# Kernel optimization log

Hardware: AMD Instinct MI355X
Metric: run time of the kernel (lower is better)

The kernel has to match this reference:

```python
import jax, jax.numpy as jnp
import numpy as np

B, T, S, C, E, H = 4, 2048, 2048, 256, 512, 8
D = E // H
SCALE = E ** (-0.5)


def setup_inputs() -> dict:
    key = jax.random.key(0)
    ks = jax.random.split(key, 12)
    x = jax.random.normal(ks[0], (B, T, C), dtype=jnp.float32)
    context = jax.random.normal(ks[1], (B, S, E), dtype=jnp.float32)
    pad_mask = jax.random.randint(ks[2], (B, T, S), 0, 2) == 1
    p = 0.02
    # Conv1d kernel_size=1 weights stored squeezed: [out_ch, in_ch]
    w_in = jax.random.normal(ks[3], (E, C), dtype=jnp.float32) * p
    b_in = jnp.zeros((E,), dtype=jnp.float32)
    wq = jax.random.normal(ks[4], (E, E), dtype=jnp.float32) * p
    bq = jnp.zeros((E,), dtype=jnp.float32)
    wk = jax.random.normal(ks[5], (E, E), dtype=jnp.float32) * p
    bk = jnp.zeros((E,), dtype=jnp.float32)
    wv = jax.random.normal(ks[6], (E, E), dtype=jnp.float32) * p
    bv = jnp.zeros((E,), dtype=jnp.float32)
    w_out = jax.random.normal(ks[7], (C, E), dtype=jnp.float32) * p
    b_out = jnp.zeros((C,), dtype=jnp.float32)
    return {"x": x, "context": context, "pad_mask": pad_mask,
            "w_in": w_in, "b_in": b_in, "wq": wq, "bq": bq,
            "wk": wk, "bk": bk, "wv": wv, "bv": bv,
            "w_out": w_out, "b_out": b_out}


def reference(x, context, pad_mask, w_in, b_in, wq, bq, wk, bk, wv, bv, w_out, b_out):
    # proj_in: Conv1d k=1 == per-token linear on channel dim. [B,T,C] -> [B,T,E]
    xe = jnp.einsum('btc,ec->bte', x, w_in) + b_in
    Q = (xe @ wq.T + bq).reshape(B, T, H, D)       # query tokens
    K = (context @ wk.T + bk).reshape(B, S, H, D)  # key tokens
    V = (context @ wv.T + bv).reshape(B, S, H, D)
    att = jnp.einsum('bihd,bjhd->bhij', Q, K) * SCALE  # [B,H,T,S]
    att = jnp.where(pad_mask[:, None, :, :], jnp.float32(-1e9), att)
    att = jax.nn.softmax(att, axis=-1)
    out = jnp.einsum('bhij,bjhd->bihd', att, V).reshape(B, T, E)
    # proj_out: Conv1d k=1, [B,T,E] -> [B,T,C]
    out = jnp.einsum('bte,ce->btc', out, w_out) + b_out
    return out
```

## Files before the change

### kernel.cpp

```cpp
#include <hip/hip_runtime.h>
#include <cstdint>
#include <cstddef>

#define Bb 4
#define Tt 2048
#define Ssz 2048
#define Cc 256
#define Ee 512
#define Hh 8

typedef short bf8 __attribute__((ext_vector_type(8)));
typedef float f4 __attribute__((ext_vector_type(4)));
typedef float f16v __attribute__((ext_vector_type(16)));
typedef unsigned int u32x2 __attribute__((ext_vector_type(2)));
typedef unsigned int u32x4 __attribute__((ext_vector_type(4)));

__device__ __forceinline__ unsigned short f2bf(float x) {
  unsigned int u = __float_as_uint(x);
  u += 0x7fffu + ((u >> 16) & 1u);
  return (unsigned short)(u >> 16);
}

__device__ __forceinline__ bf8 cvt8(float4 a, float4 b) {
  bf8 r;
  r[0] = (short)f2bf(a.x); r[1] = (short)f2bf(a.y);
  r[2] = (short)f2bf(a.z); r[3] = (short)f2bf(a.w);
  r[4] = (short)f2bf(b.x); r[5] = (short)f2bf(b.y);
  r[6] = (short)f2bf(b.z); r[7] = (short)f2bf(b.w);
  return r;
}

#if __has_builtin(__builtin_amdgcn_perm)
#define PACK2(u0, u1) __builtin_amdgcn_perm((u1), (u0), 0x07060302u)
#else
#define PACK2(u0, u1) (((u0) >> 16) | ((u1) & 0xffff0000u))
#endif

#define EXPU(v) __float_as_uint(__builtin_amdgcn_exp2f(v))
#define MFMA32(a, b, c) __builtin_amdgcn_mfma_f32_32x32x16_bf16((a), (b), (c), 0, 0, 0)

__device__ __forceinline__ void pl32swap(unsigned int& a, unsigned int& b) {
#if __has_builtin(__builtin_amdgcn_permlane32_swap)
  u32x2 r = __builtin_amdgcn_permlane32_swap(a, b, false, false);
  a = r[0];
  b = r[1];
#else
  unsigned int ax = (unsigned int)__shfl_xor((int)a, 32);
  unsigned int bx = (unsigned int)__shfl_xor((int)b, 32);
  bool hi = (threadIdx.x & 32) != 0;
  unsigned int an = hi ? bx : a;
  unsigned int bn = hi ? b : ax;
  a = an;
  b = bn;
#endif
}

__global__ __launch_bounds__(256) void prep(const float* __restrict__ w_in,
                                            const float* __restrict__ b_in,
                                            const float* __restrict__ wq,
                                            const float* __restrict__ bq,
                                            const float* __restrict__ wk,
                                            const float* __restrict__ wv,
                                            const float* __restrict__ wo,
                                            unsigned short* __restrict__ wkvb,
                                            unsigned short* __restrict__ wob,
                                            unsigned short* __restrict__ wqin,
                                            float* __restrict__ bqinb, float qsc) {
  __shared__ unsigned short sh[128][72];
  const int bid = blockIdx.x, tid = threadIdx.x;
  if (bid < 512) {
    int i = bid * 256 + tid;
    const float* s = (i < 65536) ? wk : wv;
    int off = (i < 65536) ? i : i - 65536;
    float4 v = ((const float4*)s)[off];
    ushort4 o;
    o.x = f2bf(v.x); o.y = f2bf(v.y); o.z = f2bf(v.z); o.w = f2bf(v.w);
    ((ushort4*)wkvb)[i] = o;
  } else if (bid < 640) {
    int i = (bid - 512) * 256 + tid;
    float4 v = ((const float4*)wo)[i];
    ushort4 o;
    o.x = f2bf(v.x); o.y = f2bf(v.y); o.z = f2bf(v.z); o.w = f2bf(v.w);
    ((ushort4*)wob)[i] = o;
  } else if (bid < 672) {
    const int idx = bid - 640;
    const int m0 = (idx & 7) * 64, n0 = (idx >> 3) * 64;
    unsigned short (*As)[72] = (unsigned short (*)[72]) & sh[0][0];
    unsigned short (*Bs)[72] = (unsigned short (*)[72]) & sh[64][0];
    const int wave = tid >> 6, lane = tid & 63;
    const int lrow = lane & 15, quad = lane >> 4;
    const int wm = (wave >> 1) * 32, wn = (wave & 1) * 32;
    const int arow = tid >> 3, ac = tid & 7;
    f4 acc[2][2];
#pragma unroll
    for (int i = 0; i < 2; i++)
#pragma unroll
      for (int j = 0; j < 2; j++) {
        f4 z = {0.f, 0.f, 0.f, 0.f};
        acc[i][j] = z;
      }
    for (int kt = 0; kt < 8; kt++) {
#pragma unroll
      for (int i = 0; i < 2; i++) {
        int row = arow + i * 32;
        const float* src = wq + (size_t)(m0 + row) * Ee + kt * 64 + ac * 8;
        float4 v0 = *(const float4*)src, v1 = *(const float4*)(src + 4);
        bf8 av;
        av[0] = (short)f2bf(v0.x * qsc); av[1] = (short)f2bf(v0.y * qsc);
        av[2] = (short)f2bf(v0.z * qsc); av[3] = (short)f2bf(v0.w * qsc);
        av[4] = (short)f2bf(v1.x * qsc); av[5] = (short)f2bf(v1.y * qsc);
        av[6] = (short)f2bf(v1.z * qsc); av[7] = (short)f2bf(v1.w * qsc);
        *(bf8*)&As[row][ac * 8] = av;
        int c = n0 + row;
        bf8 bv;
#pragma unroll
        for (int k = 0; k < 8; k++)
          bv[k] = (short)f2bf(w_in[(size_t)(kt * 64 + ac * 8 + k) * Cc + c]);
        *(bf8*)&Bs[row][ac * 8] = bv;
      }
      __syncthreads();
#pragma unroll
      for (int kk = 0; kk < 2; kk++) {
        bf8 af[2], bff[2];
#pragma unroll
        for (int i = 0; i < 2; i++) af[i] = *(const bf8*)&As[wm + i * 16 + lrow][kk * 32 + quad * 8];
#pragma unroll
        for (int j = 0; j < 2; j++) bff[j] = *(const bf8*)&Bs[wn + j * 16 + lrow][kk * 32 + quad * 8];
#pragma unroll
        for (int i = 0; i < 2; i++)
#pragma unroll
          for (int j = 0; j < 2; j++)
            acc[i][j] = __builtin_amdgcn_mfma_f32_16x16x32_bf16(af[i], bff[j], acc[i][j], 0, 0, 0);
      }
      __syncthreads();
    }
#pragma unroll
    for (int j = 0; j < 2; j++)
#pragma unroll
      for (int i = 0; i < 2; i++)
#pragma unroll
        for (int r = 0; r < 4; r++)
          wqin[(size_t)(m0 + wm + i * 16 + quad * 4 + r) * Cc + n0 + wn + j * 16 + lrow] =
              f2bf(acc[i][j][r]);
  } else {
    const int o = (bid - 672) * 32 + (tid >> 3);
    const int k0 = (tid & 7) * 64;
    float s = 0.f;
#pragma unroll
    for (int i = 0; i < 16; i++) {
      float4 w = *(const float4*)(wq + (size_t)o * Ee + k0 + i * 4);
      float4 bb = *(const float4*)(b_in + k0 + i * 4);
      s += w.x * bb.x + w.y * bb.y + w.z * bb.z + w.w * bb.w;
    }
    s += __shfl_xor(s, 1);
    s += __shfl_xor(s, 2);
    s += __shfl_xor(s, 4);
    if ((tid & 7) == 0) bqinb[o] = (s + bq[o]) * qsc;
  }
}

__global__ __launch_bounds__(256) void qkv(const float* __restrict__ x,
                                           const float* __restrict__ ctx,
                                           const unsigned short* __restrict__ wqin,
                                           const float* __restrict__ bqinb,
                                           const unsigned short* __restrict__ wkv,
                                           const float* __restrict__ bk,
                                           const float* __restrict__ bv,
                                           unsigned short* __restrict__ Qb,
                                           unsigned short* __restrict__ Kb,
                                           unsigned short* __restrict__ Vt,
                                           const int* __restrict__ mask,
                                           unsigned int* __restrict__ mp) {
  __shared__ unsigned short As[128][72];
  __shared__ unsigned short Bs[128][72];
  const int bid = blockIdx.x, tid = threadIdx.x;
  if (bid >= 768) {
    int i = (bid - 768) * 256 + tid;
    const int4* src = (const int4*)mask + (size_t)i * 8;
    unsigned int w = 0;
#pragma unroll
    for (int k = 0; k < 8; k++) {
      int4 v = src[k];
      w |= (unsigned int)(v.x != 0) << (k * 4);
      w |= (unsigned int)(v.y != 0) << (k * 4 + 1);
      w |= (unsigned int)(v.z != 0) << (k * 4 + 2);
      w |= (unsigned int)(v.w != 0) << (k * 4 + 3);
    }
    mp[i] = w;
    return;
  }
  const bool isQ = bid < 256;
  const int idx = isQ ? bid : bid - 256;
  const int m0 = (idx & 63) * 128;
  const int n0 = (idx >> 6) * 128;
  const int K = isQ ? 256 : 512;
  const float* A = isQ ? x : ctx;
  const unsigned short* Bt = isQ ? wqin : wkv;

  const int wave = tid >> 6, lane = tid & 63;
  const int lrow = lane & 15, quad = lane >> 4;
  const int wm = (wave >> 1) * 64, wn = (wave & 1) * 64;
  const int arow = tid >> 3, ac = tid & 7;

  f4 acc[4][4];
#pragma unroll
  for (int i = 0; i < 4; i++)
#pragma unroll
    for (int j = 0; j < 4; j++) {
      f4 z = {0.f, 0.f, 0.f, 0.f};
      acc[i][j] = z;
    }

  float4 ap0[4], ap1[4];
  bf8 bpre[4];
#pragma unroll
  for (int i = 0; i < 4; i++) {
    const float* src = A + (size_t)(m0 + arow + i * 32) * K + ac * 8;
    ap0[i] = *(const float4*)src;
    ap1[i] = *(const float4*)(src + 4);
    bpre[i] = *(const bf8*)(Bt + (size_t)(n0 + arow + i * 32) * K + ac * 8);
  }

  const int nkt = K >> 6;
  for (int kt = 0; kt < nkt; ++kt) {
#pragma unroll
    for (int i = 0; i < 4; i++) {
      *(bf8*)&As[arow + i * 32][ac * 8] = cvt8(ap0[i], ap1[i]);
      *(bf8*)&Bs[arow + i * 32][ac * 8] = bpre[i];
    }
    __syncthreads();
    if (kt + 1 < nkt) {
      int k0 = (kt + 1) << 6;
#pragma unroll
      for (int i = 0; i < 4; i++) {
        const float* src = A + (size_t)(m0 + arow + i * 32) * K + k0 + ac * 8;
        ap0[i] = *(const float4*)src;
        ap1[i] = *(const float4*)(src + 4);
        bpre[i] = *(const bf8*)(Bt + (size_t)(n0 + arow + i * 32) * K + k0 + ac * 8);
      }
    }
#pragma unroll
    for (int kk = 0; kk < 2; kk++) {
      bf8 af[4], bff[4];
#pragma unroll
      for (int i = 0; i < 4; i++)
        af[i] = *(const bf8*)&As[wm + i * 16 + lrow][kk * 32 + quad * 8];
#pragma unroll
      for (int j = 0; j < 4; j++)
        bff[j] = *(const bf8*)&Bs[wn + j * 16 + lrow][kk * 32 + quad * 8];
#pragma unroll
      for (int i = 0; i < 4; i++)
#pragma unroll
        for (int j = 0; j < 4; j++)
          acc[i][j] = __builtin_amdgcn_mfma_f32_16x16x32_bf16(af[i], bff[j],
                                                              acc[i][j], 0, 0, 0);
    }
    __syncthreads();
  }

  if (isQ) {
#pragma unroll
    for (int j = 0; j < 4; j++) {
      int col = n0 + wn + j * 16 + lrow;
      float bvv = bqinb[col];
#pragma unroll
      for (int i = 0; i < 4; i++)
#pragma unroll
        for (int r = 0; r < 4; r++)
          Qb[(size_t)(m0 + wm + i * 16 + quad * 4 + r) * Ee + col] =
              f2bf(acc[i][j][r] + bvv);
    }
  } else if (n0 < 512) {
#pragma unroll
    for (int j = 0; j < 4; j++) {
      int col = n0 + wn + j * 16 + lrow;
      float bvv = bk[col];
#pragma unroll
      for (int i = 0; i < 4; i++)
#pragma unroll
        for (int r = 0; r < 4; r++)
          Kb[(size_t)(m0 + wm + i * 16 + quad * 4 + r) * Ee + col] =
              f2bf(acc[i][j][r] + bvv);
    }
  } else {
#pragma unroll
    for (int j = 0; j < 4; j++) {
      int d = n0 - 512 + wn + j * 16 + lrow;
      int h = d >> 6, dd = d & 63;
      float bvv = bv[d];
#pragma unroll
      for (int i = 0; i < 4; i++) {
        int tok = m0 + wm + i * 16 + quad * 4;
        int b = tok >> 11, sl = tok & 2047;
        ushort4 pk;
        pk.x = f2bf(acc[i][j][0] + bvv);
        pk.y = f2bf(acc[i][j][1] + bvv);
        pk.z = f2bf(acc[i][j][2] + bvv);
        pk.w = f2bf(acc[i][j][3] + bvv);
        *(ushort4*)(Vt + (size_t)((b * Hh + h) * 64 + dd) * Ssz + sl) = pk;
      }
    }
  }
}

template <bool OUT_BF16, int BM, int BN, int WGM>
__global__ __launch_bounds__(256) void gemm_bt(const unsigned short* __restrict__ A,
                                               const unsigned short* __restrict__ Bt,
                                               const float* __restrict__ bias0,
                                               void* __restrict__ Cout,
                                               int M, int N, int K) {
  constexpr int WGN = 4 / WGM;
  constexpr int MI = BM / (WGM * 16);
  constexpr int NJ = BN / (WGN * 16);
  constexpr int NA = BM / 32;
  constexpr int NB = BN / 32;
  __shared__ unsigned short As[BM][72];
  __shared__ unsigned short Bs[BN][72];
  const int tid = threadIdx.x;
  const int wave = tid >> 6, lane = tid & 63;
  const int lrow = lane & 15, quad = lane >> 4;
  const int wm = (wave / WGN) * (BM / WGM);
  const int wn = (wave % WGN) * (BN / WGN);
  const int m0 = blockIdx.x * BM, n0 = blockIdx.y * BN;
  const int arow = tid >> 3, ac = tid & 7;

  f4 acc[MI][NJ];
#pragma unroll
  for (int i = 0; i < MI; i++)
#pragma unroll
    for (int j = 0; j < NJ; j++) {
      f4 z = {0.f, 0.f, 0.f, 0.f};
      acc[i][j] = z;
    }

  bf8 apre[NA], bpre[NB];
#pragma unroll
  for (int i = 0; i < NA; i++)
    apre[i] = *(const bf8*)(A + (size_t)(m0 + arow + i * 32) * K + ac * 8);
#pragma unroll
  for (int i = 0; i < NB; i++)
    bpre[i] = *(const bf8*)(Bt + (size_t)(n0 + arow + i * 32) * K + ac * 8);

  const int nkt = K >> 6;
  for (int kt = 0; kt < nkt; ++kt) {
#pragma unroll
    for (int i = 0; i < NA; i++) *(bf8*)&As[arow + i * 32][ac * 8] = apre[i];
#pragma unroll
    for (int i = 0; i < NB; i++) *(bf8*)&Bs[arow + i * 32][ac * 8] = bpre[i];
    __syncthreads();
    if (kt + 1 < nkt) {
      int k0 = (kt + 1) << 6;
#pragma unroll
      for (int i = 0; i < NA; i++)
        apre[i] = *(const bf8*)(A + (size_t)(m0 + arow + i * 32) * K + k0 + ac * 8);
#pragma unroll
      for (int i = 0; i < NB; i++)
        bpre[i] = *(const bf8*)(Bt + (size_t)(n0 + arow + i * 32) * K + k0 + ac * 8);
    }
#pragma unroll
    for (int kk = 0; kk < 2; kk++) {
      bf8 af[MI], bff[NJ];
#pragma unroll
      for (int i = 0; i < MI; i++)
        af[i] = *(const bf8*)&As[wm + i * 16 + lrow][kk * 32 + quad * 8];
#pragma unroll
      for (int j = 0; j < NJ; j++)
        bff[j] = *(const bf8*)&Bs[wn + j * 16 + lrow][kk * 32 + quad * 8];
#pragma unroll
      for (int i = 0; i < MI; i++)
#pragma unroll
        for (int j = 0; j < NJ; j++)
          acc[i][j] = __builtin_amdgcn_mfma_f32_16x16x32_bf16(af[i], bff[j],
                                                              acc[i][j], 0, 0, 0);
    }
    __syncthreads();
  }

#pragma unroll
  for (int j = 0; j < NJ; j++) {
    int col = n0 + wn + j * 16 + lrow;
    float bvv = bias0 ? bias0[col] : 0.f;
#pragma unroll
    for (int i = 0; i < MI; i++) {
#pragma unroll
      for (int r = 0; r < 4; r++) {
        int row = m0 + wm + i * 16 + quad * 4 + r;
        float v = acc[i][j][r] + bvv;
        if (OUT_BF16)
          ((unsigned short*)Cout)[(size_t)row * N + col] = f2bf(v);
        else
          ((float*)Cout)[(size_t)row * N + col] = v;
      }
    }
  }
}

__global__ __launch_bounds__(256, 2) void attn(const unsigned short* __restrict__ Q,
                                               const unsigned short* __restrict__ K,
                                               const unsigned short* __restrict__ Vt,
                                               const unsigned int* __restrict__ mp,
                                               unsigned short* __restrict__ O) {
  __shared__ unsigned short Ks[2][64][72];
  __shared__ unsigned short Vts[2][64][72];
  const int tid = threadIdx.x;
  const int wave = tid >> 6, lane = tid & 63;
  const int l31 = lane & 31, hi = lane >> 5;
  const int bid = blockIdx.x;
  const int bh = bid & 31, b = bh >> 3, h = bh & 7;
  const int t0 = (bid >> 5) * 128;
  const int wm = wave * 32;
  const int arow = tid >> 3, ac = tid & 7;

  const unsigned short* Qrow =
      Q + (size_t)(b * Tt + t0 + wm + l31) * Ee + h * 64 + hi * 8;
  bf8 qf[4];
#pragma unroll
  for (int c = 0; c < 4; c++) qf[c] = *(const bf8*)(Qrow + c * 16);

  f16v oacc0, oacc1, dacc;
#pragma unroll
  for (int r = 0; r < 16; r++) {
    oacc0[r] = 0.f;
    oacc1[r] = 0.f;
    dacc[r] = 0.f;
  }
  bf8 ones;
#pragma unroll
  for (int k = 0; k < 8; k++) ones[k] = (short)0x3F80;

  const unsigned short* Kbase = K + (size_t)b * Ssz * Ee + h * 64;
  const unsigned short* Vbase = Vt + (size_t)((b * Hh + h) * 64) * Ssz;
  const unsigned int* mroww = mp + (size_t)(b * Tt + t0 + wm + l31) * 64;

  bf8 kreg[2], vreg[2];
#pragma unroll
  for (int i = 0; i < 2; i++) {
    int row = arow + i * 32;
    kreg[i] = *(const bf8*)(Kbase + (size_t)row * Ee + ac * 8);
    vreg[i] = *(const bf8*)(Vbase + (size_t)row * Ssz + ac * 8);
  }
#pragma unroll
  for (int i = 0; i < 2; i++) {
    int row = arow + i * 32;
    *(bf8*)&Ks[0][row][ac * 8] = kreg[i];
    *(bf8*)&Vts[0][row][ac * 8] = vreg[i];
  }
  __syncthreads();

  for (int n = 0; n < 32; n++) {
    const int s0 = n * 64;
    const int cur = n & 1;
    if (n + 1 < 32) {
#pragma unroll
      for (int i = 0; i < 2; i++) {
        int row = arow + i * 32;
        kreg[i] = *(const bf8*)(Kbase + (size_t)(s0 + 64 + row) * Ee + ac * 8);
        vreg[i] = *(const bf8*)(Vbase + (size_t)row * Ssz + s0 + 64 + ac * 8);
      }
    }
    const uint2 mw = *(const uint2*)(mroww + (s0 >> 5));
    const unsigned int wsh0 = mw.x >> (4 * hi);
    const unsigned int wsh1 = mw.y >> (4 * hi);

    f16v sa0, sa1;
#pragma unroll
    for (int r = 0; r < 16; r++) {
      const int sh = (r & 3) + 8 * (r >> 2);
      sa0[r] = ((wsh0 >> sh) & 1u) ? -1e9f : 0.f;
      sa1[r] = ((wsh1 >> sh) & 1u) ? -1e9f : 0.f;
    }
#pragma unroll
    for (int c = 0; c < 4; c++) {
      bf8 kf0 = *(const bf8*)&Ks[cur][l31][c * 16 + hi * 8];
      bf8 kf1 = *(const bf8*)&Ks[cur][32 + l31][c * 16 + hi * 8];
      sa0 = MFMA32(kf0, qf[c], sa0);
      sa1 = MFMA32(kf1, qf[c], sa1);
    }
    unsigned int X0[8], X1[8];
#pragma unroll
    for (int m = 0; m < 8; m++) {
      X0[m] = PACK2(EXPU(sa0[2 * m]), EXPU(sa0[2 * m + 1]));
      X1[m] = PACK2(EXPU(sa1[2 * m]), EXPU(sa1[2 * m + 1]));
    }
#pragma unroll
    for (int c = 0; c < 4; c++) {
      const int m0 = 4 * (c & 1);
      unsigned int a0, a1, a2, a3;
      if (c < 2) {
        a0 = X0[m0]; a1 = X0[m0 + 1]; a2 = X0[m0 + 2]; a3 = X0[m0 + 3];
      } else {
        a0 = X1[m0]; a1 = X1[m0 + 1]; a2 = X1[m0 + 2]; a3 = X1[m0 + 3];
      }
      pl32swap(a0, a2);
      pl32swap(a1, a3);
      u32x4 pdv;
      pdv[0] = a0; pdv[1] = a1; pdv[2] = a2; pdv[3] = a3;
      bf8 pa = *(bf8*)&pdv;
      bf8 vf0 = *(const bf8*)&Vts[cur][l31][c * 16 + hi * 8];
      bf8 vf1 = *(const bf8*)&Vts[cur][32 + l31][c * 16 + hi * 8];
      dacc = MFMA32(pa, ones, dacc);
      oacc0 = MFMA32(pa, vf0, oacc0);
      oacc1 = MFMA32(pa, vf1, oacc1);
    }
    if (n + 1 < 32) {
#pragma unroll
      for (int i = 0; i < 2; i++) {
        int row = arow + i * 32;
        *(bf8*)&Ks[cur ^ 1][row][ac * 8] = kreg[i];
        *(bf8*)&Vts[cur ^ 1][row][ac * 8] = vreg[i];
      }
    }
    __syncthreads();
  }

#pragma unroll
  for (int r = 0; r < 16; r++) {
    const int tl = (r & 3) + 8 * (r >> 2) + 4 * hi;
    const float inv = 1.0f / dacc[r];
    const size_t off = (size_t)(b * Tt + t0 + wm + tl) * Ee + h * 64 + l31;
    O[off] = f2bf(oacc0[r] * inv);
    O[off + 32] = f2bf(oacc1[r] * inv);
  }
}

extern "C" void kernel_launch(void* const* d_in, const int* in_sizes, int n_in,
                              void* d_out, int out_size, void* d_ws, size_t ws_size,
                              hipStream_t stream) {
  const float* x    = (const float*)d_in[0];
  const float* ctx  = (const float*)d_in[1];
  const int*   mask = (const int*)d_in[2];
  const float* w_in = (const float*)d_in[3];
  const float* b_in = (const float*)d_in[4];
  const float* wq   = (const float*)d_in[5];
  const float* bq   = (const float*)d_in[6];
  const float* wk   = (const float*)d_in[7];
  const float* bk   = (const float*)d_in[8];
  const float* wv   = (const float*)d_in[9];
  const float* bv   = (const float*)d_in[10];
  const float* wo   = (const float*)d_in[11];
  const float* bo   = (const float*)d_in[12];

  const float qsc = 0.04419417382415922f * 1.4426950408889634f;

  unsigned short* ws = (unsigned short*)d_ws;
  unsigned int*   maskp = (unsigned int*)ws;
  unsigned short* wkvb  = ws + 1048576;
  unsigned short* wob   = ws + 1572864;
  unsigned short* wqin  = ws + 1703936;
  float*          bqinb = (float*)(ws + 1835008);
  unsigned short* Qb    = ws + 1836032;
  unsigned short* Kb    = ws + 6030336;
  unsigned short* Vtb   = ws + 10224640;
  unsigned short* Ob    = ws + 14418944;

  prep<<<688, 256, 0, stream>>>(w_in, b_in, wq, bq, wk, wv, wo,
                                wkvb, wob, wqin, bqinb, qsc);
  qkv<<<2816, 256, 0, stream>>>(x, ctx, wqin, bqinb, wkvb, bk, bv, Qb, Kb, Vtb,
                                mask, maskp);
  attn<<<512, 256, 0, stream>>>(Qb, Kb, Vtb, maskp, Ob);
  gemm_bt<false, 64, 64, 2><<<dim3(128, 4), 256, 0, stream>>>(
      Ob, wob, bo, d_out, 8192, 256, 512);
}
```

Before: 228.3 us.

## Split attention key range across two wave groups and merge partial sums

The attention kernel now launches 512 threads per block. Two groups of four waves each process half of the key sequence, using separate double-buffered shared tiles. At the end, one group writes its unnormalized output and denominator partials to shared memory, and the other group adds them before normalizing and storing. This doubles the waves available per block to hide latency over the same 512-block grid, at the cost of more shared memory per block and an extra reduction step. The merge is valid because the softmax has no running max: the exp values are summed directly.

```diff
diff --git a/kernel.cpp b/kernel.cpp
--- a/kernel.cpp
+++ b/kernel.cpp
@@ -395,24 +395,30 @@
   }
 }
 
-__global__ __launch_bounds__(256, 2) void attn(const unsigned short* __restrict__ Q,
+__global__ __launch_bounds__(512, 2) void attn(const unsigned short* __restrict__ Q,
                                                const unsigned short* __restrict__ K,
                                                const unsigned short* __restrict__ Vt,
                                                const unsigned int* __restrict__ mp,
                                                unsigned short* __restrict__ O) {
-  __shared__ unsigned short Ks[2][64][72];
-  __shared__ unsigned short Vts[2][64][72];
+  __shared__ __align__(16) unsigned char smem[73728];
   const int tid = threadIdx.x;
   const int wave = tid >> 6, lane = tid & 63;
   const int l31 = lane & 31, hi = lane >> 5;
+  const int wsub = wave & 3, grp = wave >> 2;
   const int bid = blockIdx.x;
   const int bh = bid & 31, b = bh >> 3, h = bh & 7;
   const int t0 = (bid >> 5) * 128;
-  const int wm = wave * 32;
-  const int arow = tid >> 3, ac = tid & 7;
+  const int tw = t0 + wsub * 32;
+  const int sbase = grp << 10;
+  const int gtid = tid & 255;
+  const int arow = gtid >> 3, ac = gtid & 7;
+
+  typedef unsigned short tile2_t[2][64][72];
+  tile2_t& Ks = *(tile2_t*)(smem + grp * 36864);
+  tile2_t& Vts = *(tile2_t*)(smem + grp * 36864 + 18432);
 
   const unsigned short* Qrow =
-      Q + (size_t)(b * Tt + t0 + wm + l31) * Ee + h * 64 + hi * 8;
+      Q + (size_t)(b * Tt + tw + l31) * Ee + h * 64 + hi * 8;
   bf8 qf[4];
 #pragma unroll
   for (int c = 0; c < 4; c++) qf[c] = *(const bf8*)(Qrow + c * 16);
@@ -428,9 +434,10 @@
 #pragma unroll
   for (int k = 0; k < 8; k++) ones[k] = (short)0x3F80;
 
-  const unsigned short* Kbase = K + (size_t)b * Ssz * Ee + h * 64;
-  const unsigned short* Vbase = Vt + (size_t)((b * Hh + h) * 64) * Ssz;
-  const unsigned int* mroww = mp + (size_t)(b * Tt + t0 + wm + l31) * 64;
+  const unsigned short* Kbase = K + ((size_t)b * Ssz + sbase) * Ee + h * 64;
+  const unsigned short* Vbase = Vt + (size_t)((b * Hh + h) * 64) * Ssz + sbase;
+  const unsigned int* mroww =
+      mp + (size_t)(b * Tt + tw + l31) * 64 + (sbase >> 5);
 
   bf8 kreg[2], vreg[2];
 #pragma unroll
@@ -447,10 +454,10 @@
   }
   __syncthreads();
 
-  for (int n = 0; n < 32; n++) {
+  for (int n = 0; n < 16; n++) {
     const int s0 = n * 64;
     const int cur = n & 1;
-    if (n + 1 < 32) {
+    if (n + 1 < 16) {
 #pragma unroll
       for (int i = 0; i < 2; i++) {
         int row = arow + i * 32;
@@ -465,9 +472,9 @@
     f16v sa0, sa1;
 #pragma unroll
     for (int r = 0; r < 16; r++) {
-      const int sh = (r & 3) + 8 * (r >> 2);
-      sa0[r] = ((wsh0 >> sh) & 1u) ? -1e9f : 0.f;
-      sa1[r] = ((wsh1 >> sh) & 1u) ? -1e9f : 0.f;
+      const int shft = (r & 3) + 8 * (r >> 2);
+      sa0[r] = ((wsh0 >> shft) & 1u) ? -1e9f : 0.f;
+      sa1[r] = ((wsh1 >> shft) & 1u) ? -1e9f : 0.f;
     }
 #pragma unroll
     for (int c = 0; c < 4; c++) {
@@ -502,7 +509,7 @@
       oacc0 = MFMA32(pa, vf0, oacc0);
       oacc1 = MFMA32(pa, vf1, oacc1);
     }
-    if (n + 1 < 32) {
+    if (n + 1 < 16) {
 #pragma unroll
       for (int i = 0; i < 2; i++) {
         int row = arow + i * 32;
@@ -513,13 +520,28 @@
     __syncthreads();
   }
 
-#pragma unroll
-  for (int r = 0; r < 16; r++) {
-    const int tl = (r & 3) + 8 * (r >> 2) + 4 * hi;
-    const float inv = 1.0f / dacc[r];
-    const size_t off = (size_t)(b * Tt + t0 + wm + tl) * Ee + h * 64 + l31;
-    O[off] = f2bf(oacc0[r] * inv);
-    O[off + 32] = f2bf(oacc1[r] * inv);
+  float (*mbuf)[64][48] = (float (*)[64][48])smem;
+  if (grp) {
+#pragma unroll
+    for (int q = 0; q < 4; q++) {
+      float4 v0 = {oacc0[4 * q], oacc0[4 * q + 1], oacc0[4 * q + 2], oacc0[4 * q + 3]};
+      float4 v1 = {oacc1[4 * q], oacc1[4 * q + 1], oacc1[4 * q + 2], oacc1[4 * q + 3]};
+      float4 v2 = {dacc[4 * q], dacc[4 * q + 1], dacc[4 * q + 2], dacc[4 * q + 3]};
+      *(float4*)&mbuf[wsub][lane][4 * q] = v0;
+      *(float4*)&mbuf[wsub][lane][16 + 4 * q] = v1;
+      *(float4*)&mbuf[wsub][lane][32 + 4 * q] = v2;
+    }
+  }
+  __syncthreads();
+  if (!grp) {
+#pragma unroll
+    for (int r = 0; r < 16; r++) {
+      const int tl = (r & 3) + 8 * (r >> 2) + 4 * hi;
+      const float inv = 1.0f / (dacc[r] + mbuf[wsub][lane][32 + r]);
+      const size_t off = (size_t)(b * Tt + tw + tl) * Ee + h * 64 + l31;
+      O[off] = f2bf((oacc0[r] + mbuf[wsub][lane][r]) * inv);
+      O[off + 32] = f2bf((oacc1[r] + mbuf[wsub][lane][16 + r]) * inv);
+    }
   }
 }
 
@@ -557,7 +579,7 @@
                                 wkvb, wob, wqin, bqinb, qsc);
   qkv<<<2816, 256, 0, stream>>>(x, ctx, wqin, bqinb, wkvb, bk, bv, Qb, Kb, Vtb,
                                 mask, maskp);
-  attn<<<512, 256, 0, stream>>>(Qb, Kb, Vtb, maskp, Ob);
+  attn<<<512, 512, 0, stream>>>(Qb, Kb, Vtb, maskp, Ob);
   gemm_bt<false, 64, 64, 2><<<dim3(128, 4), 256, 0, stream>>>(
       Ob, wob, bo, d_out, 8192, 256, 512);
 }
```

Result: slower. 239.6 us (+5.0%).

## Software-pipeline QK^T one tile ahead of PV in attention loop

Applied to the files above, without the earlier changes.

Restructures the attention main loop so the QK^T MFMAs for tile n+1 are issued right after the PV MFMAs for tile n. Exponentiation then overlaps with matrix work, and K is prefetched two tiles ahead while V is prefetched one tile ahead. Wave priority is raised around the MFMA block with s_setprio. This adds register pressure from the live next-tile score accumulators and the pa fragments, which could lower occupancy.

```diff
diff --git a/kernel.cpp b/kernel.cpp
--- a/kernel.cpp
+++ b/kernel.cpp
@@ -433,6 +433,7 @@
   const unsigned int* mroww = mp + (size_t)(b * Tt + t0 + wm + l31) * 64;
 
   bf8 kreg[2], vreg[2];
+
 #pragma unroll
   for (int i = 0; i < 2; i++) {
     int row = arow + i * 32;
@@ -445,43 +446,56 @@
     *(bf8*)&Ks[0][row][ac * 8] = kreg[i];
     *(bf8*)&Vts[0][row][ac * 8] = vreg[i];
   }
+#pragma unroll
+  for (int i = 0; i < 2; i++) {
+    int row = arow + i * 32;
+    kreg[i] = *(const bf8*)(Kbase + (size_t)(64 + row) * Ee + ac * 8);
+  }
   __syncthreads();
-
-  for (int n = 0; n < 32; n++) {
-    const int s0 = n * 64;
-    const int cur = n & 1;
-    if (n + 1 < 32) {
-#pragma unroll
-      for (int i = 0; i < 2; i++) {
-        int row = arow + i * 32;
-        kreg[i] = *(const bf8*)(Kbase + (size_t)(s0 + 64 + row) * Ee + ac * 8);
-        vreg[i] = *(const bf8*)(Vbase + (size_t)row * Ssz + s0 + 64 + ac * 8);
-      }
-    }
-    const uint2 mw = *(const uint2*)(mroww + (s0 >> 5));
-    const unsigned int wsh0 = mw.x >> (4 * hi);
-    const unsigned int wsh1 = mw.y >> (4 * hi);
-
-    f16v sa0, sa1;
+#pragma unroll
+  for (int i = 0; i < 2; i++) *(bf8*)&Ks[1][arow + i * 32][ac * 8] = kreg[i];
+  f16v sa0, sa1;
+  {
+    const uint2 mw = *(const uint2*)(mroww);
+    const unsigned int w0 = mw.x >> (4 * hi);
+    const unsigned int w1 = mw.y >> (4 * hi);
 #pragma unroll
     for (int r = 0; r < 16; r++) {
       const int sh = (r & 3) + 8 * (r >> 2);
-      sa0[r] = ((wsh0 >> sh) & 1u) ? -1e9f : 0.f;
-      sa1[r] = ((wsh1 >> sh) & 1u) ? -1e9f : 0.f;
+      sa0[r] = ((w0 >> sh) & 1u) ? -1e9f : 0.f;
+      sa1[r] = ((w1 >> sh) & 1u) ? -1e9f : 0.f;
     }
 #pragma unroll
     for (int c = 0; c < 4; c++) {
-      bf8 kf0 = *(const bf8*)&Ks[cur][l31][c * 16 + hi * 8];
-      bf8 kf1 = *(const bf8*)&Ks[cur][32 + l31][c * 16 + hi * 8];
+      bf8 kf0 = *(const bf8*)&Ks[0][l31][c * 16 + hi * 8];
+      bf8 kf1 = *(const bf8*)&Ks[0][32 + l31][c * 16 + hi * 8];
       sa0 = MFMA32(kf0, qf[c], sa0);
       sa1 = MFMA32(kf1, qf[c], sa1);
     }
+  }
+  __syncthreads();
+
+  for (int n = 0; n < 32; n++) {
+    const bool more = (n + 1 < 32);
+    if (n + 2 < 32) {
+#pragma unroll
+      for (int i = 0; i < 2; i++)
+        kreg[i] = *(const bf8*)(Kbase + (size_t)((n + 2) * 64 + arow + i * 32) * Ee + ac * 8);
+    }
+    if (more) {
+#pragma unroll
+      for (int i = 0; i < 2; i++)
+        vreg[i] = *(const bf8*)(Vbase + (size_t)(arow + i * 32) * Ssz + (n + 1) * 64 + ac * 8);
+    }
+    uint2 mwn;
+    if (more) mwn = *(const uint2*)(mroww + ((n + 1) << 1));
     unsigned int X0[8], X1[8];
 #pragma unroll
     for (int m = 0; m < 8; m++) {
       X0[m] = PACK2(EXPU(sa0[2 * m]), EXPU(sa0[2 * m + 1]));
       X1[m] = PACK2(EXPU(sa1[2 * m]), EXPU(sa1[2 * m + 1]));
     }
+    bf8 pa[4];
 #pragma unroll
     for (int c = 0; c < 4; c++) {
       const int m0 = 4 * (c & 1);
@@ -495,20 +509,46 @@
       pl32swap(a1, a3);
       u32x4 pdv;
       pdv[0] = a0; pdv[1] = a1; pdv[2] = a2; pdv[3] = a3;
-      bf8 pa = *(bf8*)&pdv;
-      bf8 vf0 = *(const bf8*)&Vts[cur][l31][c * 16 + hi * 8];
-      bf8 vf1 = *(const bf8*)&Vts[cur][32 + l31][c * 16 + hi * 8];
-      dacc = MFMA32(pa, ones, dacc);
-      oacc0 = MFMA32(pa, vf0, oacc0);
-      oacc1 = MFMA32(pa, vf1, oacc1);
-    }
-    if (n + 1 < 32) {
-#pragma unroll
-      for (int i = 0; i < 2; i++) {
-        int row = arow + i * 32;
-        *(bf8*)&Ks[cur ^ 1][row][ac * 8] = kreg[i];
-        *(bf8*)&Vts[cur ^ 1][row][ac * 8] = vreg[i];
-      }
+      pa[c] = *(bf8*)&pdv;
+    }
+    if (more) {
+      const unsigned int w0 = mwn.x >> (4 * hi);
+      const unsigned int w1 = mwn.y >> (4 * hi);
+#pragma unroll
+      for (int r = 0; r < 16; r++) {
+        const int sh = (r & 3) + 8 * (r >> 2);
+        sa0[r] = ((w0 >> sh) & 1u) ? -1e9f : 0.f;
+        sa1[r] = ((w1 >> sh) & 1u) ? -1e9f : 0.f;
+      }
+    }
+    __builtin_amdgcn_s_setprio(1);
+#pragma unroll
+    for (int c = 0; c < 4; c++) {
+      bf8 vf0 = *(const bf8*)&Vts[n & 1][l31][c * 16 + hi * 8];
+      bf8 vf1 = *(const bf8*)&Vts[n & 1][32 + l31][c * 16 + hi * 8];
+      dacc = MFMA32(pa[c], ones, dacc);
+      oacc0 = MFMA32(pa[c], vf0, oacc0);
+      oacc1 = MFMA32(pa[c], vf1, oacc1);
+    }
+    if (more) {
+#pragma unroll
+      for (int c = 0; c < 4; c++) {
+        bf8 kf0 = *(const bf8*)&Ks[(n + 1) & 1][l31][c * 16 + hi * 8];
+        bf8 kf1 = *(const bf8*)&Ks[(n + 1) & 1][32 + l31][c * 16 + hi * 8];
+        sa0 = MFMA32(kf0, qf[c], sa0);
+        sa1 = MFMA32(kf1, qf[c], sa1);
+      }
+    }
+    __builtin_amdgcn_s_setprio(0);
+    if (more) {
+#pragma unroll
+      for (int i = 0; i < 2; i++)
+        *(bf8*)&Vts[(n + 1) & 1][arow + i * 32][ac * 8] = vreg[i];
+    }
+    if (n + 2 < 32) {
+#pragma unroll
+      for (int i = 0; i < 2; i++)
+        *(bf8*)&Ks[n & 1][arow + i * 32][ac * 8] = kreg[i];
     }
     __syncthreads();
   }
```

After: 230.0 us. Within noise of the previous version (+0.8%).
